# Performance work log

Hardware: AMD Instinct MI355X
Metric: run time of the kernel (lower is better)

## Reference

```python
import jax, jax.numpy as jnp
import numpy as np

INPUT_WIDTH = 256
DEPTH = 7
OUTPUT_WIDTH = 256
N_NODES = 2 ** (DEPTH + 1) - 1  # 255


def setup_inputs() -> dict:
    key = jax.random.key(0)
    k_x, k_w1, k_w2 = jax.random.split(key, 3)
    init1 = 1.0 / np.sqrt(INPUT_WIDTH)
    x = jax.random.normal(k_x, (2, 1024, INPUT_WIDTH), dtype=jnp.float32)
    w1s = jax.random.uniform(k_w1, (N_NODES, INPUT_WIDTH), jnp.float32, -init1, init1)
    b1s = jnp.zeros((N_NODES,), jnp.float32)
    w2s = jax.random.uniform(k_w2, (N_NODES, INPUT_WIDTH, OUTPUT_WIDTH), jnp.float32, -init1, init1)
    b2s = jnp.zeros((N_NODES, OUTPUT_WIDTH), jnp.float32)
    return {"x": x, "w1s": w1s, "b1s": b1s, "w2s": w2s, "b2s": b2s}


def reference(x, w1s, b1s, w2s, b2s):
    B, S, D = x.shape
    flat_x = x.reshape(B * S, D)  # [T, D]
    T = flat_x.shape[0]

    # --- routing pass: walk the binary tree, recording node ids and logits ---
    current = jnp.zeros((T,), dtype=jnp.int32)
    all_nodes = []
    all_logits = []
    for _ in range(DEPTH + 1):
        all_nodes.append(current)
        score = jnp.einsum('td,td->t', flat_x, w1s[current]) + b1s[current]  # [T]
        all_logits.append(score)
        # ((sign+1)/2).long(): sign(0)->0 maps to choice 0 via truncation
        choice = ((jnp.sign(score) + 1.0) / 2.0).astype(jnp.int32)
        current = current * 2 + choice + 1

    logits = jnp.stack(all_logits, axis=1)  # [T, DEPTH+1]
    path_weights = jax.nn.gelu(jnp.abs(logits), approximate=False)  # exact erf GELU

    # --- output pass: weighted sum of per-node transforms along the path ---
    out = jnp.zeros((T, OUTPUT_WIDTH), dtype=x.dtype)
    for i in range(DEPTH + 1):
        nodes_i = all_nodes[i]
        t_i = jnp.einsum('td,tdo->to', flat_x, w2s[nodes_i]) + b2s[nodes_i]  # [T, O]
        out = out + t_i * path_weights[:, i][:, None]

    return out.reshape(B, S, OUTPUT_WIDTH)
```

## Files before the change

kernel.cpp:

```cpp
#include <hip/hip_runtime.h>
#include <hip/hip_bf16.h>

#define T_TOKENS 2048
#define DIM 256
#define NLEV 8
#define MAXU 512

using bf16x8 = __attribute__((ext_vector_type(8))) short;
using f32x4  = __attribute__((ext_vector_type(4))) float;

__device__ __forceinline__ unsigned short f2bf(float f) {
    union { float f; unsigned u; } v; v.f = f;
    unsigned r = v.u + 0x7FFFu + ((v.u >> 16) & 1u);
    return (unsigned short)(r >> 16);
}
__device__ __forceinline__ float bf2f(unsigned short h) {
    union { unsigned u; float f; } w; w.u = (unsigned)h << 16; return w.f;
}

__global__ __launch_bounds__(256) void route_kernel(
    const float* __restrict__ x, const float* __restrict__ w1s,
    const float* __restrict__ b1s,
    float* __restrict__ pw, int* __restrict__ pc,
    unsigned short* __restrict__ xbf)
{
    int wave = threadIdx.x >> 6;
    int lane = threadIdx.x & 63;
    int t = blockIdx.x * 4 + wave;

    const float4 xv = *reinterpret_cast<const float4*>(x + (size_t)t * DIM + lane * 4);

    ushort4 xb;
    xb.x = f2bf(xv.x); xb.y = f2bf(xv.y); xb.z = f2bf(xv.z); xb.w = f2bf(xv.w);
    *reinterpret_cast<ushort4*>(xbf + (size_t)t * DIM + lane * 4) = xb;

    int p = 1;
    float keep = 0.0f;
    #pragma unroll
    for (int lvl = 0; lvl < NLEV; ++lvl) {
        int node = p - 1;
        const float4 wv = *reinterpret_cast<const float4*>(w1s + (size_t)node * DIM + lane * 4);
        float s = xv.x * wv.x + xv.y * wv.y + xv.z * wv.z + xv.w * wv.w;
        #pragma unroll
        for (int off = 32; off; off >>= 1) s += __shfl_xor(s, off);
        float score = s + b1s[node];
        float a = fabsf(score);
        float g = a * 0.5f * (1.0f + erff(a * 0.70710678118654752f));
        if (lane == lvl) keep = g;
        int choice = (score > 0.0f) ? 1 : 0;
        p = 2 * p + choice;
    }
    if (lane < NLEV) pw[(size_t)t * NLEV + lane] = keep;
    if (lane == 0) pc[t] = p;
}

__global__ __launch_bounds__(256) void sort_kernel(
    const int* __restrict__ pc,
    int* __restrict__ order, unsigned* __restrict__ units, int* __restrict__ ucount)
{
    __shared__ int hist[256];
    __shared__ int offs[256];
    __shared__ int cums[257];
    __shared__ int wpart[4];
    int tid = threadIdx.x;
    hist[tid] = 0;
    __syncthreads();

    int myPc[8];
    #pragma unroll
    for (int i = 0; i < 8; ++i) {
        int t = tid * 8 + i;
        myPc[i] = pc[t];
        atomicAdd(&hist[myPc[i] - 256], 1);
    }
    __syncthreads();

    if (tid < 64) {
        int lane = tid;
        int v0 = hist[lane * 4 + 0], v1 = hist[lane * 4 + 1];
        int v2 = hist[lane * 4 + 2], v3 = hist[lane * 4 + 3];
        int sum = v0 + v1 + v2 + v3;
        int scan = sum;
        #pragma unroll
        for (int off = 1; off < 64; off <<= 1) {
            int n = __shfl_up(scan, off);
            if (lane >= off) scan += n;
        }
        int excl = scan - sum;
        offs[lane * 4 + 0] = excl;
        offs[lane * 4 + 1] = excl + v0;
        offs[lane * 4 + 2] = excl + v0 + v1;
        offs[lane * 4 + 3] = excl + v0 + v1 + v2;
    }
    __syncthreads();

    cums[tid] = offs[tid];
    if (tid == 0) cums[256] = T_TOKENS;
    __syncthreads();

    #pragma unroll
    for (int i = 0; i < 8; ++i) {
        int t = tid * 8 + i;
        int bin = myPc[i] - 256;
        int pos = atomicAdd(&offs[bin], 1);
        order[pos] = t;
    }

    int nch = 0, s = 0, e = 0, l = 0;
    if (tid < 255) {
        int q = tid + 1;
        l = 31 - __clz(q);
        int shift = 8 - l;
        int lo = (q << shift) - 256;
        int hi = ((q + 1) << shift) - 256;
        s = cums[lo];
        e = cums[hi];
        nch = (e - s + 63) >> 6;
    }
    int lane = tid & 63, w = tid >> 6;
    int scan = nch;
    #pragma unroll
    for (int off = 1; off < 64; off <<= 1) {
        int n = __shfl_up(scan, off);
        if (lane >= off) scan += n;
    }
    if (lane == 63) wpart[w] = scan;
    __syncthreads();
    int pre = 0;
    for (int k = 0; k < w; ++k) pre += wpart[k];
    int base = pre + scan - nch;
    for (int j = 0; j < nch; ++j) {
        int st = s + j * 64;
        int c = e - st; if (c > 64) c = 64;
        units[base + j] = (unsigned)tid | ((unsigned)l << 8) |
                          ((unsigned)st << 11) | ((unsigned)c << 22);
    }
    if (tid == 255) *ucount = pre + scan;
}

__global__ __launch_bounds__(256, 4) void out_kernel(
    const unsigned short* __restrict__ xbf, const float* __restrict__ w2s,
    const float* __restrict__ b2s, const float* __restrict__ pw,
    const int* __restrict__ order, const unsigned* __restrict__ units,
    const int* __restrict__ ucount, unsigned short* __restrict__ lvlbuf)
{
    __shared__ float Bs[2][32][128];

    int bid = blockIdx.x;
    int L = (bid & 7) * 128 + (bid >> 3);
    int u = L >> 1;
    int ch = L & 1;
    if (u >= *ucount) return;
    unsigned d = units[u];
    int node  = (int)(d & 255u);
    int lvl   = (int)((d >> 8) & 7u);
    int start = (int)((d >> 11) & 2047u);
    int cnt   = (int)((d >> 22) & 127u);

    int tid = threadIdx.x;
    int wv = tid >> 6, lane = tid & 63;
    int l15 = lane & 15, kg = lane >> 4;

    int tok[4];
    #pragma unroll
    for (int m = 0; m < 4; ++m) {
        int r = m * 16 + l15;
        tok[m] = order[start + (r < cnt ? r : cnt - 1)];
    }

    const float* w2n = w2s + ((size_t)node << 16) + ch * 128;
    int srow = wv * 8 + (lane >> 5);
    int scol = (lane & 31) * 4;

    auto STAGE = [&](int p, int q) {
        #pragma unroll
        for (int i = 0; i < 4; ++i) {
            const float* src = w2n + (size_t)(p * 32 + srow + i * 2) * 256 + scol;
            float* dst = &Bs[q][wv * 8 + i * 2][0];
            __builtin_amdgcn_global_load_lds(
                (const __attribute__((address_space(1))) void*)src,
                (__attribute__((address_space(3))) void*)dst, 16, 0, 0);
        }
    };
    auto LOADA = [&](int p, bf16x8 (&a)[4]) {
        #pragma unroll
        for (int m = 0; m < 4; ++m)
            a[m] = *reinterpret_cast<const bf16x8*>(xbf + ((size_t)tok[m] << 8) + p * 32 + kg * 8);
    };

    f32x4 acc[4][2];
    #pragma unroll
    for (int m = 0; m < 4; ++m) {
        acc[m][0] = (f32x4){0.f, 0.f, 0.f, 0.f};
        acc[m][1] = (f32x4){0.f, 0.f, 0.f, 0.f};
    }

    auto COMPUTE = [&](int q, const bf16x8 (&a)[4]) {
        bf16x8 bf[2];
        #pragma unroll
        for (int nb = 0; nb < 2; ++nb) {
            bf16x8 v;
            #pragma unroll
            for (int i = 0; i < 8; ++i)
                v[i] = (short)f2bf(Bs[q][kg * 8 + i][wv * 32 + nb * 16 + l15]);
            bf[nb] = v;
        }
        #pragma unroll
        for (int m = 0; m < 4; ++m) if (m * 16 < cnt)
            #pragma unroll
            for (int nb = 0; nb < 2; ++nb)
                acc[m][nb] = __builtin_amdgcn_mfma_f32_16x16x32_bf16(a[m], bf[nb], acc[m][nb], 0, 0, 0);
    };

    bf16x8 aP[4], aQ[4];

    STAGE(0, 0);
    LOADA(0, aP);
    STAGE(1, 1);
    asm volatile("s_waitcnt vmcnt(4)" ::: "memory");
    __builtin_amdgcn_s_barrier();
    __builtin_amdgcn_sched_barrier(0);

    #pragma unroll
    for (int p = 0; p < 8; ++p) {
        if (p & 1) COMPUTE(1, aQ); else COMPUTE(0, aP);
        __builtin_amdgcn_s_barrier();
        if (p < 6) {
            if (p & 1) LOADA(p + 1, aP); else LOADA(p + 1, aQ);
            STAGE(p + 2, p & 1);
            asm volatile("s_waitcnt vmcnt(4)" ::: "memory");
        } else if (p == 6) {
            LOADA(7, aQ);
            asm volatile("s_waitcnt vmcnt(0)" ::: "memory");
        }
        __builtin_amdgcn_s_barrier();
        __builtin_amdgcn_sched_barrier(0);
    }

    float bias[2];
    #pragma unroll
    for (int nb = 0; nb < 2; ++nb)
        bias[nb] = b2s[((size_t)node << 8) + ch * 128 + wv * 32 + nb * 16 + l15];

    unsigned short* dst = lvlbuf + ((size_t)lvl << 19);

    #pragma unroll
    for (int m = 0; m < 4; ++m) if (m * 16 < cnt) {
        #pragma unroll
        for (int j = 0; j < 4; ++j) {
            int r = m * 16 + kg * 4 + j;
            if (r < cnt) {
                int t = __shfl(tok[m], kg * 4 + j);
                float w = pw[(size_t)t * NLEV + lvl];
                #pragma unroll
                for (int nb = 0; nb < 2; ++nb)
                    dst[((size_t)t << 8) + ch * 128 + wv * 32 + nb * 16 + l15] =
                        f2bf(w * (acc[m][nb][j] + bias[nb]));
            }
        }
    }
}

__global__ __launch_bounds__(256) void reduce_kernel(
    const unsigned short* __restrict__ lvlbuf, float* __restrict__ out)
{
    int idx = blockIdx.x * 256 + threadIdx.x;
    const ushort4* lb = reinterpret_cast<const ushort4*>(lvlbuf);
    float4 s = {0.f, 0.f, 0.f, 0.f};
    #pragma unroll
    for (int l = 0; l < NLEV; ++l) {
        ushort4 v = lb[(size_t)l * 131072 + idx];
        s.x += bf2f(v.x); s.y += bf2f(v.y); s.z += bf2f(v.z); s.w += bf2f(v.w);
    }
    reinterpret_cast<float4*>(out)[idx] = s;
}

extern "C" void kernel_launch(void* const* d_in, const int* in_sizes, int n_in,
                              void* d_out, int out_size, void* d_ws, size_t ws_size,
                              hipStream_t stream) {
    const float* x   = (const float*)d_in[0];
    const float* w1s = (const float*)d_in[1];
    const float* b1s = (const float*)d_in[2];
    const float* w2s = (const float*)d_in[3];
    const float* b2s = (const float*)d_in[4];
    float* out = (float*)d_out;

    float* pw            = (float*)d_ws;
    int* pc              = (int*)(pw + T_TOKENS * NLEV);
    int* order           = pc + T_TOKENS;
    unsigned* units      = (unsigned*)(order + T_TOKENS);
    int* ucount          = (int*)(units + MAXU);
    unsigned short* xbf  = (unsigned short*)((char*)d_ws + (256 << 10));
    unsigned short* lvlbuf = (unsigned short*)((char*)d_ws + (2 << 20));

    route_kernel<<<T_TOKENS / 4, 256, 0, stream>>>(x, w1s, b1s, pw, pc, xbf);
    sort_kernel<<<1, 256, 0, stream>>>(pc, order, units, ucount);
    out_kernel<<<2 * MAXU, 256, 0, stream>>>(xbf, w2s, b2s, pw, order, units, ucount, lvlbuf);
    reduce_kernel<<<512, 256, 0, stream>>>(lvlbuf, out);
}
```

Baseline: 46.15 us.

## Deepen out_kernel pipeline to four LDS stages with prefetch distance three

Changes the output GEMM kernel from a 2-stage to a 4-stage LDS ring buffer. Weight tiles and activation fragments are now prefetched three steps ahead, with graded vmcnt waits. LDS use doubles and the launch bound drops to 2 blocks per CU. The block-index swizzle across units is also removed, so units map linearly to blocks. This trades occupancy for more memory latency hiding.

```diff
diff --git a/kernel.cpp b/kernel.cpp
--- a/kernel.cpp
+++ b/kernel.cpp
@@ -138,24 +138,22 @@
     if (tid == 255) *ucount = pre + scan;
 }
 
-__global__ __launch_bounds__(256, 4) void out_kernel(
+__global__ __launch_bounds__(256, 2) void out_kernel(
     const unsigned short* __restrict__ xbf, const float* __restrict__ w2s,
     const float* __restrict__ b2s, const float* __restrict__ pw,
     const int* __restrict__ order, const unsigned* __restrict__ units,
     const int* __restrict__ ucount, unsigned short* __restrict__ lvlbuf)
 {
-    __shared__ float Bs[2][32][128];
-
-    int bid = blockIdx.x;
-    int L = (bid & 7) * 128 + (bid >> 3);
-    int u = L >> 1;
-    int ch = L & 1;
+    __shared__ float Bs[4][32][128];
+
+    int u = blockIdx.x >> 1;
     if (u >= *ucount) return;
     unsigned d = units[u];
     int node  = (int)(d & 255u);
     int lvl   = (int)((d >> 8) & 7u);
     int start = (int)((d >> 11) & 2047u);
     int cnt   = (int)((d >> 22) & 127u);
+    int ch = blockIdx.x & 1;
 
     int tid = threadIdx.x;
     int wv = tid >> 6, lane = tid & 63;
@@ -212,29 +210,35 @@
                 acc[m][nb] = __builtin_amdgcn_mfma_f32_16x16x32_bf16(a[m], bf[nb], acc[m][nb], 0, 0, 0);
     };
 
-    bf16x8 aP[4], aQ[4];
-
-    STAGE(0, 0);
-    LOADA(0, aP);
-    STAGE(1, 1);
-    asm volatile("s_waitcnt vmcnt(4)" ::: "memory");
-    __builtin_amdgcn_s_barrier();
-    __builtin_amdgcn_sched_barrier(0);
+    bf16x8 a0[4], a1[4], a2[4], a3[4];
+
+    STAGE(0, 0); LOADA(0, a0);
+    STAGE(1, 1); LOADA(1, a1);
+    STAGE(2, 2); LOADA(2, a2);
 
     #pragma unroll
     for (int p = 0; p < 8; ++p) {
-        if (p & 1) COMPUTE(1, aQ); else COMPUTE(0, aP);
-        __builtin_amdgcn_s_barrier();
-        if (p < 6) {
-            if (p & 1) LOADA(p + 1, aP); else LOADA(p + 1, aQ);
-            STAGE(p + 2, p & 1);
-            asm volatile("s_waitcnt vmcnt(4)" ::: "memory");
-        } else if (p == 6) {
-            LOADA(7, aQ);
-            asm volatile("s_waitcnt vmcnt(0)" ::: "memory");
-        }
+        if (p < 6)       asm volatile("s_waitcnt vmcnt(16)" ::: "memory");
+        else if (p == 6) asm volatile("s_waitcnt vmcnt(8)" ::: "memory");
+        else             asm volatile("s_waitcnt vmcnt(0)" ::: "memory");
         __builtin_amdgcn_s_barrier();
         __builtin_amdgcn_sched_barrier(0);
+
+        if ((p & 3) == 0)      COMPUTE(0, a0);
+        else if ((p & 3) == 1) COMPUTE(1, a1);
+        else if ((p & 3) == 2) COMPUTE(2, a2);
+        else                   COMPUTE(3, a3);
+
+        __builtin_amdgcn_s_barrier();
+        __builtin_amdgcn_sched_barrier(0);
+
+        if (p + 3 < 8) {
+            int q = (p + 3) & 3;
+            if (q == 0)      { STAGE(p + 3, 0); LOADA(p + 3, a0); }
+            else if (q == 1) { STAGE(p + 3, 1); LOADA(p + 3, a1); }
+            else if (q == 2) { STAGE(p + 3, 2); LOADA(p + 3, a2); }
+            else             { STAGE(p + 3, 3); LOADA(p + 3, a3); }
+        }
     }
 
     float bias[2];
```

Result: slower. 47.63 us (+3.2%).
